# Optimization experiments

Measured on AMD Instinct MI355X. Metric: run time of the kernel, lower is better.

The kernel has to match this reference:

```python
import jax, jax.numpy as jnp
import numpy as np

B, P, D = 32, 2048, 256  # batch, patch_num, input_dim


def setup_inputs() -> dict:
    key = jax.random.key(0)
    ks = jax.random.split(key, 6)
    n = lambda k, shape: jax.random.normal(k, shape, dtype=jnp.float32) * 0.02
    return {
        "x": jax.random.normal(ks[0], (B, P, D), dtype=jnp.float32),
        "mlp_w": n(ks[1], (D, D)), "mlp_b": jnp.zeros((D,), jnp.float32),
        "his_w": n(ks[2], (D, D)), "his_b": jnp.zeros((D,), jnp.float32),
        "cur_w": n(ks[3], (D, D)), "cur_b": jnp.zeros((D,), jnp.float32),
        "wl_w": n(ks[4], (D, P)), "wl_b": jnp.zeros((P,), jnp.float32),
        "gate_w": n(ks[5], (D, 1)), "gate_b": jnp.zeros((1,), jnp.float32),
        "ln_g": jnp.ones((D,), jnp.float32), "ln_b": jnp.zeros((D,), jnp.float32),
    }


def _layernorm(h, g, b, eps=1e-5):
    mu = h.mean(-1, keepdims=True)
    var = ((h - mu) ** 2).mean(-1, keepdims=True)
    return (h - mu) * jax.lax.rsqrt(var + eps) * g + b


def reference(x, mlp_w, mlp_b, his_w, his_b, cur_w, cur_b, wl_w, wl_b,
              gate_w, gate_b, ln_g, ln_b):
    origin = x
    # expert_num == 0 -> MoE branch skipped, x unchanged
    H = origin @ his_w + his_b                              # extractor_his: [B,P,D]
    # gate(extractor_cur(origin)) -> [B,P,1], repeated along last dim == broadcast
    weight_current = (origin @ cur_w + cur_b) @ gate_w + gate_b  # [B,P,1]
    logits = H @ wl_w + wl_b                                # [B,P,P]
    weight = jax.nn.softmax(logits, axis=-1)                # row softmax
    adj = jnp.tril(weight)                                  # causal mask (diagonal=0)
    aggregated = jnp.einsum('bpq,bqd->bpd', adj, origin)    # [B,P,D]
    H_history = aggregated @ mlp_w + mlp_b                  # dropout is identity (p=0)
    H_current = weight_current * origin
    out = _layernorm(H_history + H_current, ln_g, ln_b)     # aggregated_norm == 1
    return (out, origin)
```

## Files before the change

### kernel.cpp

```cpp
#include <hip/hip_runtime.h>
#include <hip/hip_bf16.h>

typedef __attribute__((ext_vector_type(8))) short s8v;
typedef __attribute__((ext_vector_type(4))) float f4v;
typedef __attribute__((ext_vector_type(4))) unsigned int u4v;

#define BATCH 32
#define SEQ   2048
#define DIM   256
#define ORIGIN_OFF ((size_t)BATCH * SEQ * DIM)

#define XT_OFF  0ull
#define WL_OFF  16777216ull
#define HIS_OFF 17301504ull
#define MLP_OFF 17367040ull

#define BK0   0
#define BK1   32768
#define BX0   65536
#define BX1   98304
#define EP_CG 69632
#define EP_CB 70656
#define EP_WP 70672
#define EP_WC 72720

__device__ __forceinline__ unsigned short f2bf(float f) {
  __hip_bfloat16 h = __float2bfloat16(f);
  return *reinterpret_cast<unsigned short*>(&h);
}
__device__ __forceinline__ f4v mfma16(s8v a, s8v b, f4v c) {
  return __builtin_amdgcn_mfma_f32_16x16x32_bf16(a, b, c, 0, 0, 0);
}
__device__ __forceinline__ unsigned int pk2(float lo, float hi) {
  return (unsigned int)f2bf(lo) | ((unsigned int)f2bf(hi) << 16);
}
__device__ __forceinline__ void dma16(const void* g, void* l) {
  __builtin_amdgcn_global_load_lds(
      (const __attribute__((address_space(1))) unsigned int*)g,
      (__attribute__((address_space(3))) unsigned int*)l, 16, 0, 0);
}

__global__ __launch_bounds__(256) void prep_all(
    const float* __restrict__ x, const float* __restrict__ wl_w,
    const float* __restrict__ his_w, const float* __restrict__ mlp_w,
    unsigned short* __restrict__ ws)
{
  __shared__ unsigned short tile[64][72];
  const int t = threadIdx.x;
  const int tb = blockIdx.x;
  const float* src; unsigned short* dst; int lds_, ldd_, r0, c0;
  bool isx = false;
  if (tb < 4096) {
    const int b = tb >> 7, rem = tb & 127;
    r0 = (rem >> 2) * 64;  c0 = (rem & 3) * 64;
    src = x + (size_t)b * SEQ * DIM;  lds_ = DIM;
    dst = ws + XT_OFF + (size_t)b * DIM * SEQ;  ldd_ = SEQ;
    isx = true;
  } else if (tb < 4224) {
    const int t2 = tb - 4096;
    r0 = (t2 >> 5) * 64;  c0 = (t2 & 31) * 64;
    src = wl_w;  lds_ = 2048;  dst = ws + WL_OFF;  ldd_ = 256;
  } else if (tb < 4240) {
    const int t2 = tb - 4224;
    r0 = (t2 >> 2) * 64;  c0 = (t2 & 3) * 64;
    src = his_w;  lds_ = 256;  dst = ws + HIS_OFF;  ldd_ = 256;
  } else {
    const int t2 = tb - 4240;
    r0 = (t2 >> 2) * 64;  c0 = (t2 & 3) * 64;
    src = mlp_w;  lds_ = 256;  dst = ws + MLP_OFF;  ldd_ = 256;
  }
  {
    const int rr = t >> 2, cc = (t & 3) * 16;
    const float* s0 = src + (size_t)(r0 + rr) * lds_ + c0 + cc;
    f4v v0 = *(const f4v*)(s0);
    f4v v1 = *(const f4v*)(s0 + 4);
    f4v v2 = *(const f4v*)(s0 + 8);
    f4v v3 = *(const f4v*)(s0 + 12);
    u4v o0, o1;
    o0[0] = pk2(v0[0], v0[1]); o0[1] = pk2(v0[2], v0[3]);
    o0[2] = pk2(v1[0], v1[1]); o0[3] = pk2(v1[2], v1[3]);
    o1[0] = pk2(v2[0], v2[1]); o1[1] = pk2(v2[2], v2[3]);
    o1[2] = pk2(v3[0], v3[1]); o1[3] = pk2(v3[2], v3[3]);
    const int swz = rr >> 4;
    const int ch = cc >> 3;
    unsigned short* trow = &tile[rr][0];
    *(u4v*)(trow + ((ch ^ swz) << 3)) = o0;
    *(u4v*)(trow + (((ch + 1) ^ swz) << 3)) = o1;
  }
  __syncthreads();
  {
    const int cl = t >> 2, sg = t & 3;
    const int el = cl & 7;
    u4v o0, o1;
    if (isx) {
      #pragma unroll
      for (int m = 0; m < 8; ++m) {
        const int q = 32 * (sg >> 1) + 8 * (sg & 1)
                    + 16 * ((m >> 1) & 1) + 4 * (m >> 2) + 2 * (m & 1);
        const int chb = ((cl >> 3) ^ (q >> 4)) << 3;
        const unsigned int vv = (unsigned int)tile[q][chb + el]
                              | ((unsigned int)tile[q + 1][chb + el] << 16);
        if (m < 4) o0[m] = vv; else o1[m - 4] = vv;
      }
    } else {
      const int chb = ((cl >> 3) ^ sg) << 3;
      #pragma unroll
      for (int j = 0; j < 4; ++j) {
        const int rA = sg * 16 + 2 * j;
        o0[j] = (unsigned int)tile[rA][chb + el]
              | ((unsigned int)tile[rA + 1][chb + el] << 16);
      }
      #pragma unroll
      for (int j = 0; j < 4; ++j) {
        const int rA = sg * 16 + 8 + 2 * j;
        o1[j] = (unsigned int)tile[rA][chb + el]
              | ((unsigned int)tile[rA + 1][chb + el] << 16);
      }
    }
    unsigned short* d0 = dst + (size_t)(c0 + cl) * ldd_ + r0 + sg * 16;
    *(u4v*)d0 = o0;
    *(u4v*)(d0 + 8) = o1;
  }
}


__device__ __forceinline__ void gemm_stage(
    const unsigned short* __restrict__ Wt, const s8v (&af)[8],
    f4v (&acc)[16], char* smem_, int wq, int lane, int col16, int quad, int x7)
{
  char* sW = smem_ + BX1;
  const int rsub = lane >> 5;
  const int c = lane & 31;
  for (int st = 0; st < 4; ++st) {
    if (st) __syncthreads();
    #pragma unroll
    for (int j = 0; j < 4; ++j) {
      const int row = wq * 8 + 2 * j + rsub;
      dma16(Wt + (size_t)(st * 64 + row) * 256 + ((c ^ (row & 7)) << 3),
            sW + wq * 4096 + j * 1024);
    }
    __syncthreads();
    #pragma unroll
    for (int s = 0; s < 8; ++s) {
      const int co = ((s * 4 + quad) ^ x7) << 4;
      #pragma unroll
      for (int nt = 0; nt < 4; ++nt) {
        s8v bfr = *(const s8v*)(sW + (nt * 16 + col16) * 512 + co);
        acc[st * 4 + nt] = mfma16(af[s], bfr, acc[st * 4 + nt]);
      }
    }
  }
}

__global__ __launch_bounds__(512, 2)
void tfs_kernel(
    const float* __restrict__ x,
    const float* __restrict__ mlp_b,
    const float* __restrict__ his_b,
    const float* __restrict__ cur_w,
    const float* __restrict__ cur_b,
    const float* __restrict__ wl_b,
    const float* __restrict__ gate_w,
    const float* __restrict__ gate_b,
    const float* __restrict__ ln_g,
    const float* __restrict__ ln_b,
    const unsigned short* __restrict__ wsp,
    float* __restrict__ out)
{
  __shared__ __align__(16) char smem[131072];

  const int tid = threadIdx.x;
  const int lane = tid & 63;
  const int col16 = lane & 15;
  const int quad = lane >> 4;
  const int w = tid >> 6;
  const int x7 = col16 & 7;
  const int wq = __builtin_amdgcn_readfirstlane(w);

  const int b = blockIdx.y;
  const int pidx = (blockIdx.x + b) & 15;
  const int p0 = pidx * 128;
  const int pw = p0 + w * 16;
  const int pmax_qi = (p0 + 127) >> 6;

  const float* xb = x + (size_t)b * SEQ * DIM;
  const unsigned short* wlT  = wsp + WL_OFF;
  const unsigned short* hisT = wsp + HIS_OFF;
  const unsigned short* mlpT = wsp + MLP_OFF;
  const unsigned short* xTb  = wsp + XT_OFF + (size_t)b * DIM * SEQ;
  const f4v zero4 = {0.f, 0.f, 0.f, 0.f};

  s8v xf[8];
  {
    const float* srcx = xb + (size_t)(pw + col16) * DIM;
    #pragma unroll
    for (int s = 0; s < 8; ++s) {
      const int k0 = (s * 4 + quad) * 8;
      f4v v0 = *(const f4v*)(srcx + k0);
      f4v v1 = *(const f4v*)(srcx + k0 + 4);
      u4v o;
      o[0] = pk2(v0[0], v0[1]); o[1] = pk2(v0[2], v0[3]);
      o[2] = pk2(v1[0], v1[1]); o[3] = pk2(v1[2], v1[3]);
      xf[s] = *(s8v*)&o;
    }
  }

  f4v accQ[16];
  #pragma unroll
  for (int i = 0; i < 16; ++i) accQ[i] = zero4;
  gemm_stage(hisT, xf, accQ, smem, wq, lane, col16, quad, x7);
  #pragma unroll
  for (int i = 0; i < 16; ++i) {
    const int n = (i >> 2) * 64 + (i & 3) * 16 + col16;
    const float bias = his_b[n];
    #pragma unroll
    for (int r = 0; r < 4; ++r) {
      const int row = w * 16 + quad * 4 + r;
      *(unsigned short*)(smem + row * 528 + n * 2) = f2bf(accQ[i][r] + bias);
    }
  }
  __syncthreads();
  s8v qf[8];
  #pragma unroll
  for (int s = 0; s < 8; ++s)
    qf[s] = *(const s8v*)(smem + (w * 16 + col16) * 528 + (s * 4 + quad) * 16);
  __syncthreads();

  {
    const int rsub = lane >> 5, c = lane & 31;
    #pragma unroll
    for (int j = 0; j < 4; ++j) {
      const int row = wq * 8 + 2 * j + rsub;
      dma16(wlT + ((size_t)row << 8) + ((c ^ (row & 7)) << 3),
            smem + BK0 + wq * 4096 + j * 1024);
    }
    const int dsub = lane >> 3, cx = lane & 7;
    #pragma unroll
    for (int j = 0; j < 4; ++j) {
      const int d = wq * 32 + 8 * j + dsub;
      dma16(xTb + ((size_t)d << 11) + ((cx ^ dsub) << 3),
            smem + BX0 + wq * 4096 + j * 1024);
    }
  }
  __syncthreads();

  f4v accO[16];
  #pragma unroll
  for (int dt = 0; dt < 16; ++dt) accO[dt] = zero4;
  float mrun = -1.0e30f, Zrun = 0.f;

  #pragma unroll 1
  for (int qi = 0; qi < 32; ++qi) {
    const int q0 = qi * 64;
    char* bK = smem + BK0 + ((qi & 1) << 15);
    char* bX = smem + BX0 + ((qi & 1) << 15);
    char* nK = smem + BK0 + ((~qi & 1) << 15);
    char* nX = smem + BX0 + ((~qi & 1) << 15);

    if (qi < 31) {
      const int rsub = lane >> 5, c = lane & 31;
      #pragma unroll
      for (int j = 0; j < 4; ++j) {
        const int row = wq * 8 + 2 * j + rsub;
        dma16(wlT + ((size_t)(q0 + 64 + row) << 8) + ((c ^ (row & 7)) << 3),
              nK + wq * 4096 + j * 1024);
      }
      if (qi + 1 <= pmax_qi) {
        const int dsub = lane >> 3, cx = lane & 7;
        #pragma unroll
        for (int j = 0; j < 4; ++j) {
          const int d = wq * 32 + 8 * j + dsub;
          dma16(xTb + ((size_t)d << 11) + (q0 + 64) + ((cx ^ dsub) << 3),
                nX + wq * 4096 + j * 1024);
        }
      }
    }

    f4v accST[4];
    accST[0] = zero4; accST[1] = zero4; accST[2] = zero4; accST[3] = zero4;
    #pragma unroll
    for (int s = 0; s < 8; ++s) {
      const int co = ((s * 4 + quad) ^ x7) << 4;
      #pragma unroll
      for (int t = 0; t < 4; ++t) {
        s8v kf = *(const s8v*)(bK + (t * 16 + col16) * 512 + co);
        accST[t] = mfma16(kf, qf[s], accST[t]);
      }
    }
    #pragma unroll
    for (int t = 0; t < 4; ++t) {
      const f4v wb = *(const f4v*)(wl_b + q0 + t * 16 + quad * 4);
      #pragma unroll
      for (int r = 0; r < 4; ++r) accST[t][r] += wb[r];
    }
    float m01 = fmaxf(fmaxf(accST[0][0], accST[0][1]), fmaxf(accST[0][2], accST[0][3]));
    float m23 = fmaxf(fmaxf(accST[1][0], accST[1][1]), fmaxf(accST[1][2], accST[1][3]));
    float m45 = fmaxf(fmaxf(accST[2][0], accST[2][1]), fmaxf(accST[2][2], accST[2][3]));
    float m67 = fmaxf(fmaxf(accST[3][0], accST[3][1]), fmaxf(accST[3][2], accST[3][3]));
    float mt = fmaxf(fmaxf(m01, m23), fmaxf(m45, m67));
    mt = fmaxf(mt, __shfl_xor(mt, 16, 64));
    mt = fmaxf(mt, __shfl_xor(mt, 32, 64));
    const int grow = (mt > mrun) ? 1 : 0;
    const float mnew = fmaxf(mrun, mt);
    float Pv[4][4];
    #pragma unroll
    for (int t = 0; t < 4; ++t)
      #pragma unroll
      for (int r = 0; r < 4; ++r)
        Pv[t][r] = __expf(fminf(accST[t][r] - mnew, 0.f));
    float rs = 0.f;
    #pragma unroll
    for (int t = 0; t < 4; ++t)
      rs += (Pv[t][0] + Pv[t][1]) + (Pv[t][2] + Pv[t][3]);
    rs += __shfl_xor(rs, 16, 64);
    rs += __shfl_xor(rs, 32, 64);

    if (__any(grow)) {
      const float alpha = __expf(fminf(mrun - mnew, 0.f));
      float aO[4];
      #pragma unroll
      for (int r = 0; r < 4; ++r) aO[r] = __shfl(alpha, quad * 4 + r, 64);
      #pragma unroll
      for (int dt = 0; dt < 16; ++dt)
        #pragma unroll
        for (int r = 0; r < 4; ++r) accO[dt][r] *= aO[r];
      Zrun = Zrun * alpha + rs;
    } else {
      Zrun += rs;
    }
    mrun = mnew;

    if (q0 <= pw + 15) {
      const int lim = pw + col16 - q0;
      float Pm[4][4];
      #pragma unroll
      for (int t = 0; t < 4; ++t)
        #pragma unroll
        for (int r = 0; r < 4; ++r) {
          const int q = t * 16 + quad * 4 + r;
          Pm[t][r] = (q <= lim) ? Pv[t][r] : 0.f;
        }
      #pragma unroll
      for (int h = 0; h < 2; ++h) {
        u4v pw4;
        pw4[0] = pk2(Pm[2 * h][0], Pm[2 * h][1]);
        pw4[1] = pk2(Pm[2 * h][2], Pm[2 * h][3]);
        pw4[2] = pk2(Pm[2 * h + 1][0], Pm[2 * h + 1][1]);
        pw4[3] = pk2(Pm[2 * h + 1][2], Pm[2 * h + 1][3]);
        s8v pa = *(s8v*)&pw4;
        const int co = ((h * 4 + quad) ^ x7) << 4;
        #pragma unroll
        for (int dt = 0; dt < 16; ++dt) {
          const int d = dt * 16 + col16;
          s8v bv = *(const s8v*)(bX + d * 128 + co);
          accO[dt] = mfma16(pa, bv, accO[dt]);
        }
      }
    }
    __syncthreads();
  }

  float invZO[4];
  #pragma unroll
  for (int r = 0; r < 4; ++r) {
    const float z = __shfl(Zrun, quad * 4 + r, 64);
    invZO[r] = 1.0f / fmaxf(z, 1e-30f);
  }
  #pragma unroll
  for (int dt = 0; dt < 16; ++dt) {
    const int d = dt * 16 + col16;
    #pragma unroll
    for (int r = 0; r < 4; ++r) {
      const int row = w * 16 + quad * 4 + r;
      *(unsigned short*)(smem + row * 528 + d * 2) = f2bf(accO[dt][r] * invZO[r]);
    }
  }
  __syncthreads();
  s8v af[8];
  #pragma unroll
  for (int s = 0; s < 8; ++s)
    af[s] = *(const s8v*)(smem + (w * 16 + col16) * 528 + (s * 4 + quad) * 16);

  f4v accH[16];
  #pragma unroll
  for (int i = 0; i < 16; ++i) accH[i] = zero4;
  gemm_stage(mlpT, af, accH, smem, wq, lane, col16, quad, x7);

  float* cgL = (float*)(smem + EP_CG);
  float* cbL = (float*)(smem + EP_CB);
  if (tid < 256) {
    const float* cw = cur_w + (size_t)tid * DIM;
    float s = 0.f;
    #pragma unroll 8
    for (int i = 0; i < 64; ++i) {
      f4v vc = *(const f4v*)(cw + i * 4);
      f4v vg = *(const f4v*)(gate_w + i * 4);
      s += vc[0] * vg[0] + vc[1] * vg[1] + vc[2] * vg[2] + vc[3] * vg[3];
    }
    cgL[tid] = s;
    if (tid == 0) {
      float s2 = 0.f;
      for (int j = 0; j < DIM; ++j) s2 += cur_b[j] * gate_w[j];
      cbL[0] = s2 + gate_b[0];
    }
  }
  __syncthreads();

  float* wp = (float*)(smem + EP_WP);
  {
    const int row = tid >> 2, sg = tid & 3;
    const float* xr = xb + (size_t)(p0 + row) * DIM + sg * 64;
    const float* cgp = cgL + sg * 64;
    float sacc = 0.f;
    #pragma unroll
    for (int i = 0; i < 16; ++i) {
      f4v xv4 = *(const f4v*)(xr + i * 4);
      sacc += xv4[0] * cgp[i * 4] + xv4[1] * cgp[i * 4 + 1]
            + xv4[2] * cgp[i * 4 + 2] + xv4[3] * cgp[i * 4 + 3];
    }
    wp[row * 4 + sg] = sacc;
  }
  __syncthreads();
  float* wcS = (float*)(smem + EP_WC);
  if (tid < 128) {
    wcS[tid] = wp[tid * 4] + wp[tid * 4 + 1] + wp[tid * 4 + 2] + wp[tid * 4 + 3]
             + cbL[0];
  }
  __syncthreads();

  float s1l[4], s2l[4];
  #pragma unroll
  for (int r = 0; r < 4; ++r) { s1l[r] = 0.f; s2l[r] = 0.f; }
  #pragma unroll
  for (int i = 0; i < 16; ++i) {
    const int n = (i >> 2) * 64 + (i & 3) * 16 + col16;
    const float mb = mlp_b[n];
    #pragma unroll
    for (int r = 0; r < 4; ++r) {
      const int row = w * 16 + quad * 4 + r;
      const float xv = xb[(size_t)(p0 + row) * DIM + n];
      const float v = accH[i][r] + mb + wcS[row] * xv;
      accH[i][r] = v;
      s1l[r] += v;
      s2l[r] += v * v;
    }
  }
  #pragma unroll
  for (int r = 0; r < 4; ++r) {
    float v1 = s1l[r], v2 = s2l[r];
    v1 += __shfl_xor(v1, 1, 64); v2 += __shfl_xor(v2, 1, 64);
    v1 += __shfl_xor(v1, 2, 64); v2 += __shfl_xor(v2, 2, 64);
    v1 += __shfl_xor(v1, 4, 64); v2 += __shfl_xor(v2, 4, 64);
    v1 += __shfl_xor(v1, 8, 64); v2 += __shfl_xor(v2, 8, 64);
    s1l[r] = v1; s2l[r] = v2;
  }
  float mean_[4], rstd_[4];
  #pragma unroll
  for (int r = 0; r < 4; ++r) {
    const float mean = s1l[r] * (1.0f / 256.0f);
    const float var = s2l[r] * (1.0f / 256.0f) - mean * mean;
    mean_[r] = mean;
    rstd_[r] = rsqrtf(fmaxf(var, 0.f) + 1e-5f);
  }
  #pragma unroll
  for (int i = 0; i < 16; ++i) {
    const int n = (i >> 2) * 64 + (i & 3) * 16 + col16;
    const float g = ln_g[n];
    const float be = ln_b[n];
    #pragma unroll
    for (int r = 0; r < 4; ++r) {
      const int row = w * 16 + quad * 4 + r;
      const float y = (accH[i][r] - mean_[r]) * rstd_[r] * g + be;
      out[((size_t)b * SEQ + p0 + row) * DIM + n] = y;
    }
  }

  {
    const int row = tid >> 2, cs = (tid & 3) * 64;
    const float* src = xb + (size_t)(p0 + row) * DIM + cs;
    float* dst = out + ORIGIN_OFF + ((size_t)b * SEQ + p0 + row) * DIM + cs;
    #pragma unroll
    for (int j = 0; j < 16; ++j)
      *(f4v*)(dst + j * 4) = *(const f4v*)(src + j * 4);
  }
}

extern "C" void kernel_launch(void* const* d_in, const int* in_sizes, int n_in,
                              void* d_out, int out_size, void* d_ws, size_t ws_size,
                              hipStream_t stream) {
  const float* x      = (const float*)d_in[0];
  const float* mlp_w  = (const float*)d_in[1];
  const float* mlp_b  = (const float*)d_in[2];
  const float* his_w  = (const float*)d_in[3];
  const float* his_b  = (const float*)d_in[4];
  const float* cur_w  = (const float*)d_in[5];
  const float* cur_b  = (const float*)d_in[6];
  const float* wl_w   = (const float*)d_in[7];
  const float* wl_b   = (const float*)d_in[8];
  const float* gate_w = (const float*)d_in[9];
  const float* gate_b = (const float*)d_in[10];
  const float* ln_g   = (const float*)d_in[11];
  const float* ln_b   = (const float*)d_in[12];

  unsigned short* ws = (unsigned short*)d_ws;

  prep_all<<<dim3(4256), 256, 0, stream>>>(x, wl_w, his_w, mlp_w, ws);
  tfs_kernel<<<dim3(16, 32), 512, 0, stream>>>(
      x, mlp_b, his_b, cur_w, cur_b, wl_b, gate_w, gate_b,
      ln_g, ln_b, ws, (float*)d_out);
}
```

Baseline: 448.3 us.

## Defer P·X MFMA by one tile to overlap with next score MFMAs

Software-pipelines the attention-style loop. The probability fragments of each key tile are kept in registers, and their P·X MFMAs are issued in the next iteration right after the score MFMAs, with a final drain after the loop. The X tile is now loaded into the current buffer and consumed one iteration later, so the softmax-to-PV dependency no longer stalls the matrix units. In exchange it holds two extra fragment registers and adds an epilogue, and correctness relies on the deferred add happening before the running-max rescale.

```diff
diff --git a/kernel.cpp b/kernel.cpp
--- a/kernel.cpp
+++ b/kernel.cpp
@@ -234,13 +234,6 @@
       dma16(wlT + ((size_t)row << 8) + ((c ^ (row & 7)) << 3),
             smem + BK0 + wq * 4096 + j * 1024);
     }
-    const int dsub = lane >> 3, cx = lane & 7;
-    #pragma unroll
-    for (int j = 0; j < 4; ++j) {
-      const int d = wq * 32 + 8 * j + dsub;
-      dma16(xTb + ((size_t)d << 11) + ((cx ^ dsub) << 3),
-            smem + BX0 + wq * 4096 + j * 1024);
-    }
   }
   __syncthreads();
 
@@ -248,14 +241,16 @@
   #pragma unroll
   for (int dt = 0; dt < 16; ++dt) accO[dt] = zero4;
   float mrun = -1.0e30f, Zrun = 0.f;
+  s8v paA[2];
+  paA[0] = (s8v)(short)0; paA[1] = (s8v)(short)0;
 
   #pragma unroll 1
   for (int qi = 0; qi < 32; ++qi) {
     const int q0 = qi * 64;
     char* bK = smem + BK0 + ((qi & 1) << 15);
-    char* bX = smem + BX0 + ((qi & 1) << 15);
     char* nK = smem + BK0 + ((~qi & 1) << 15);
-    char* nX = smem + BX0 + ((~qi & 1) << 15);
+    char* cX = smem + BX0 + ((qi & 1) << 15);
+    char* pX = smem + BX0 + ((~qi & 1) << 15);
 
     if (qi < 31) {
       const int rsub = lane >> 5, c = lane & 31;
@@ -265,14 +260,14 @@
         dma16(wlT + ((size_t)(q0 + 64 + row) << 8) + ((c ^ (row & 7)) << 3),
               nK + wq * 4096 + j * 1024);
       }
-      if (qi + 1 <= pmax_qi) {
-        const int dsub = lane >> 3, cx = lane & 7;
-        #pragma unroll
-        for (int j = 0; j < 4; ++j) {
-          const int d = wq * 32 + 8 * j + dsub;
-          dma16(xTb + ((size_t)d << 11) + (q0 + 64) + ((cx ^ dsub) << 3),
-                nX + wq * 4096 + j * 1024);
-        }
+    }
+    if (qi <= pmax_qi) {
+      const int dsub = lane >> 3, cx = lane & 7;
+      #pragma unroll
+      for (int j = 0; j < 4; ++j) {
+        const int d = wq * 32 + 8 * j + dsub;
+        dma16(xTb + ((size_t)d << 11) + q0 + ((cx ^ dsub) << 3),
+              cX + wq * 4096 + j * 1024);
       }
     }
 
@@ -287,6 +282,20 @@
         accST[t] = mfma16(kf, qf[s], accST[t]);
       }
     }
+
+    if (qi > 0 && (q0 - 64) <= pw + 15) {
+      #pragma unroll
+      for (int h = 0; h < 2; ++h) {
+        const int co = ((h * 4 + quad) ^ x7) << 4;
+        #pragma unroll
+        for (int dt = 0; dt < 16; ++dt) {
+          const int d = dt * 16 + col16;
+          s8v bv = *(const s8v*)(pX + d * 128 + co);
+          accO[dt] = mfma16(paA[h], bv, accO[dt]);
+        }
+      }
+    }
+
     #pragma unroll
     for (int t = 0; t < 4; ++t) {
       const f4v wb = *(const f4v*)(wl_b + q0 + t * 16 + quad * 4);
@@ -347,17 +356,24 @@
         pw4[1] = pk2(Pm[2 * h][2], Pm[2 * h][3]);
         pw4[2] = pk2(Pm[2 * h + 1][0], Pm[2 * h + 1][1]);
         pw4[3] = pk2(Pm[2 * h + 1][2], Pm[2 * h + 1][3]);
-        s8v pa = *(s8v*)&pw4;
-        const int co = ((h * 4 + quad) ^ x7) << 4;
-        #pragma unroll
-        for (int dt = 0; dt < 16; ++dt) {
-          const int d = dt * 16 + col16;
-          s8v bv = *(const s8v*)(bX + d * 128 + co);
-          accO[dt] = mfma16(pa, bv, accO[dt]);
-        }
+        paA[h] = *(s8v*)&pw4;
       }
     }
     __syncthreads();
+  }
+
+  if (1984 <= pw + 15) {
+    char* pX = smem + BX0 + (1 << 15);
+    #pragma unroll
+    for (int h = 0; h < 2; ++h) {
+      const int co = ((h * 4 + quad) ^ x7) << 4;
+      #pragma unroll
+      for (int dt = 0; dt < 16; ++dt) {
+        const int d = dt * 16 + col16;
+        s8v bv = *(const s8v*)(pX + d * 128 + co);
+        accO[dt] = mfma16(paA[h], bv, accO[dt]);
+      }
+    }
   }
 
   float invZO[4];
```

New measurement: 459.5 us. 2.5% more time.

## Switch fused attention kernel to 32x32x16 MFMA with 4 waves and smaller tiles

Applied to the files above, without the earlier changes.

Replaces the 16x16x32 bf16 MFMA tiles with 32x32x16 MFMA throughout: the his and mlp GEMMs, the logits computation and the P·X accumulation. Each wave now owns 32 rows, the block drops to 256 threads, the K/X stream step shrinks from 64 to 32 columns, and LDS use halves to 64KB. The prep kernel's transposed-x layout and the LDS swizzles are reworked to match the new fragment layout. The aim is fewer MFMA issues and fewer LDS fragment reads per FLOP. The cost is more accumulator registers per thread and more loop iterations with a barrier each, so occupancy may suffer.

```diff
diff --git a/kernel.cpp b/kernel.cpp
--- a/kernel.cpp
+++ b/kernel.cpp
@@ -3,6 +3,7 @@
 
 typedef __attribute__((ext_vector_type(8))) short s8v;
 typedef __attribute__((ext_vector_type(4))) float f4v;
+typedef __attribute__((ext_vector_type(16))) float f16v;
 typedef __attribute__((ext_vector_type(4))) unsigned int u4v;
 
 #define BATCH 32
@@ -15,21 +16,18 @@
 #define HIS_OFF 17301504ull
 #define MLP_OFF 17367040ull
 
-#define BK0   0
-#define BK1   32768
-#define BX0   65536
-#define BX1   98304
-#define EP_CG 69632
-#define EP_CB 70656
-#define EP_WP 70672
-#define EP_WC 72720
+#define BX0   32768
+#define WST   32768
+#define EP_CB 1024
+#define EP_WP 1040
+#define EP_WC 2064
 
 __device__ __forceinline__ unsigned short f2bf(float f) {
   __hip_bfloat16 h = __float2bfloat16(f);
   return *reinterpret_cast<unsigned short*>(&h);
 }
-__device__ __forceinline__ f4v mfma16(s8v a, s8v b, f4v c) {
-  return __builtin_amdgcn_mfma_f32_16x16x32_bf16(a, b, c, 0, 0, 0);
+__device__ __forceinline__ f16v mfma32(s8v a, s8v b, f16v c) {
+  return __builtin_amdgcn_mfma_f32_32x32x16_bf16(a, b, c, 0, 0, 0);
 }
 __device__ __forceinline__ unsigned int pk2(float lo, float hi) {
   return (unsigned int)f2bf(lo) | ((unsigned int)f2bf(hi) << 16);
@@ -91,19 +89,24 @@
   {
     const int cl = t >> 2, sg = t & 3;
     const int el = cl & 7;
+    const int chb = ((cl >> 3) ^ sg) << 3;
     u4v o0, o1;
     if (isx) {
-      #pragma unroll
-      for (int m = 0; m < 8; ++m) {
-        const int q = 32 * (sg >> 1) + 8 * (sg & 1)
-                    + 16 * ((m >> 1) & 1) + 4 * (m >> 2) + 2 * (m & 1);
-        const int chb = ((cl >> 3) ^ (q >> 4)) << 3;
-        const unsigned int vv = (unsigned int)tile[q][chb + el]
-                              | ((unsigned int)tile[q + 1][chb + el] << 16);
-        if (m < 4) o0[m] = vv; else o1[m - 4] = vv;
+      const int pe0[4] = {0, 2, 8, 10};
+      const int pe1[4] = {4, 6, 12, 14};
+      #pragma unroll
+      for (int j = 0; j < 4; ++j) {
+        const int rA = sg * 16 + pe0[j];
+        o0[j] = (unsigned int)tile[rA][chb + el]
+              | ((unsigned int)tile[rA + 1][chb + el] << 16);
+      }
+      #pragma unroll
+      for (int j = 0; j < 4; ++j) {
+        const int rA = sg * 16 + pe1[j];
+        o1[j] = (unsigned int)tile[rA][chb + el]
+              | ((unsigned int)tile[rA + 1][chb + el] << 16);
       }
     } else {
-      const int chb = ((cl >> 3) ^ sg) << 3;
       #pragma unroll
       for (int j = 0; j < 4; ++j) {
         const int rA = sg * 16 + 2 * j;
@@ -124,35 +127,34 @@
 }
 
 
-__device__ __forceinline__ void gemm_stage(
-    const unsigned short* __restrict__ Wt, const s8v (&af)[8],
-    f4v (&acc)[16], char* smem_, int wq, int lane, int col16, int quad, int x7)
+__device__ __forceinline__ void gemm_stage32(
+    const unsigned short* __restrict__ Wt, const s8v (&af)[16],
+    f16v (&acc)[8], char* smem_, int wq, int lane)
 {
-  char* sW = smem_ + BX1;
-  const int rsub = lane >> 5;
-  const int c = lane & 31;
+  char* sW = smem_ + WST;
+  const int hi = lane >> 5, l31 = lane & 31, l7 = lane & 7;
   for (int st = 0; st < 4; ++st) {
     if (st) __syncthreads();
     #pragma unroll
-    for (int j = 0; j < 4; ++j) {
-      const int row = wq * 8 + 2 * j + rsub;
-      dma16(Wt + (size_t)(st * 64 + row) * 256 + ((c ^ (row & 7)) << 3),
-            sW + wq * 4096 + j * 1024);
+    for (int j = 0; j < 8; ++j) {
+      const int row = wq * 16 + 2 * j + hi;
+      dma16(Wt + (size_t)(st * 64 + row) * 256 + ((l31 ^ (row & 7)) << 3),
+            sW + wq * 8192 + j * 1024);
     }
     __syncthreads();
     #pragma unroll
-    for (int s = 0; s < 8; ++s) {
-      const int co = ((s * 4 + quad) ^ x7) << 4;
-      #pragma unroll
-      for (int nt = 0; nt < 4; ++nt) {
-        s8v bfr = *(const s8v*)(sW + (nt * 16 + col16) * 512 + co);
-        acc[st * 4 + nt] = mfma16(af[s], bfr, acc[st * 4 + nt]);
-      }
-    }
-  }
-}
-
-__global__ __launch_bounds__(512, 2)
+    for (int ks = 0; ks < 16; ++ks) {
+      #pragma unroll
+      for (int nt = 0; nt < 2; ++nt) {
+        s8v bfr = *(const s8v*)(sW + (nt * 32 + l31) * 512
+                                + (((ks * 2 + hi) ^ l7) << 4));
+        acc[st * 2 + nt] = mfma32(af[ks], bfr, acc[st * 2 + nt]);
+      }
+    }
+  }
+}
+
+__global__ __launch_bounds__(256, 2)
 void tfs_kernel(
     const float* __restrict__ x,
     const float* __restrict__ mlp_b,
@@ -167,228 +169,235 @@
     const unsigned short* __restrict__ wsp,
     float* __restrict__ out)
 {
-  __shared__ __align__(16) char smem[131072];
+  __shared__ __align__(16) char smem[65536];
 
   const int tid = threadIdx.x;
   const int lane = tid & 63;
-  const int col16 = lane & 15;
-  const int quad = lane >> 4;
+  const int l31 = lane & 31;
+  const int hi = lane >> 5;
+  const int l7 = lane & 7;
   const int w = tid >> 6;
-  const int x7 = col16 & 7;
   const int wq = __builtin_amdgcn_readfirstlane(w);
 
   const int b = blockIdx.y;
   const int pidx = (blockIdx.x + b) & 15;
   const int p0 = pidx * 128;
-  const int pw = p0 + w * 16;
-  const int pmax_qi = (p0 + 127) >> 6;
+  const int pw = p0 + w * 32;
+  const int pcol = pw + l31;
+  const int qimax = (p0 + 127) >> 5;
 
   const float* xb = x + (size_t)b * SEQ * DIM;
   const unsigned short* wlT  = wsp + WL_OFF;
   const unsigned short* hisT = wsp + HIS_OFF;
   const unsigned short* mlpT = wsp + MLP_OFF;
   const unsigned short* xTb  = wsp + XT_OFF + (size_t)b * DIM * SEQ;
-  const f4v zero4 = {0.f, 0.f, 0.f, 0.f};
-
-  s8v xf[8];
-  {
-    const float* srcx = xb + (size_t)(pw + col16) * DIM;
-    #pragma unroll
-    for (int s = 0; s < 8; ++s) {
-      const int k0 = (s * 4 + quad) * 8;
+
+  s8v xf[16];
+  {
+    const float* srcx = xb + (size_t)pcol * DIM;
+    #pragma unroll
+    for (int ks = 0; ks < 16; ++ks) {
+      const int k0 = ks * 16 + hi * 8;
       f4v v0 = *(const f4v*)(srcx + k0);
       f4v v1 = *(const f4v*)(srcx + k0 + 4);
       u4v o;
       o[0] = pk2(v0[0], v0[1]); o[1] = pk2(v0[2], v0[3]);
       o[2] = pk2(v1[0], v1[1]); o[3] = pk2(v1[2], v1[3]);
-      xf[s] = *(s8v*)&o;
-    }
-  }
-
-  f4v accQ[16];
-  #pragma unroll
-  for (int i = 0; i < 16; ++i) accQ[i] = zero4;
-  gemm_stage(hisT, xf, accQ, smem, wq, lane, col16, quad, x7);
-  #pragma unroll
-  for (int i = 0; i < 16; ++i) {
-    const int n = (i >> 2) * 64 + (i & 3) * 16 + col16;
+      xf[ks] = *(s8v*)&o;
+    }
+  }
+
+  f16v accQ[8];
+  #pragma unroll
+  for (int i = 0; i < 8; ++i)
+    #pragma unroll
+    for (int e = 0; e < 16; ++e) accQ[i][e] = 0.f;
+  gemm_stage32(hisT, xf, accQ, smem, wq, lane);
+  __syncthreads();
+  #pragma unroll
+  for (int i = 0; i < 8; ++i) {
+    const int n = i * 32 + l31;
     const float bias = his_b[n];
     #pragma unroll
-    for (int r = 0; r < 4; ++r) {
-      const int row = w * 16 + quad * 4 + r;
-      *(unsigned short*)(smem + row * 528 + n * 2) = f2bf(accQ[i][r] + bias);
-    }
-  }
-  __syncthreads();
-  s8v qf[8];
-  #pragma unroll
-  for (int s = 0; s < 8; ++s)
-    qf[s] = *(const s8v*)(smem + (w * 16 + col16) * 528 + (s * 4 + quad) * 16);
-  __syncthreads();
-
-  {
-    const int rsub = lane >> 5, c = lane & 31;
+    for (int r = 0; r < 16; ++r) {
+      const int ploc = w * 32 + (r & 3) + 8 * (r >> 2) + 4 * hi;
+      const int slot = (n >> 3) ^ (ploc & 7);
+      *(unsigned short*)(smem + ploc * 512 + slot * 16 + (n & 7) * 2)
+          = f2bf(accQ[i][r] + bias);
+    }
+  }
+  __syncthreads();
+  s8v qf[16];
+  #pragma unroll
+  for (int ks = 0; ks < 16; ++ks)
+    qf[ks] = *(const s8v*)(smem + (w * 32 + l31) * 512
+                           + (((ks * 2 + hi) ^ l7) << 4));
+  __syncthreads();
+
+  {
     #pragma unroll
     for (int j = 0; j < 4; ++j) {
-      const int row = wq * 8 + 2 * j + rsub;
-      dma16(wlT + ((size_t)row << 8) + ((c ^ (row & 7)) << 3),
-            smem + BK0 + wq * 4096 + j * 1024);
-    }
-    const int dsub = lane >> 3, cx = lane & 7;
+      const int q = wq * 8 + 2 * j + hi;
+      dma16(wlT + ((size_t)q << 8) + ((l31 ^ (q & 7)) << 3),
+            smem + wq * 4096 + j * 1024);
+    }
+    const int dr = lane >> 2, cx = lane & 3;
     #pragma unroll
     for (int j = 0; j < 4; ++j) {
-      const int d = wq * 32 + 8 * j + dsub;
-      dma16(xTb + ((size_t)d << 11) + ((cx ^ dsub) << 3),
+      const int d = wq * 64 + j * 16 + dr;
+      dma16(xTb + ((size_t)d << 11) + ((cx ^ ((d >> 1) & 3)) << 3),
             smem + BX0 + wq * 4096 + j * 1024);
     }
   }
   __syncthreads();
 
-  f4v accO[16];
-  #pragma unroll
-  for (int dt = 0; dt < 16; ++dt) accO[dt] = zero4;
+  f16v accO[8];
+  #pragma unroll
+  for (int dt = 0; dt < 8; ++dt)
+    #pragma unroll
+    for (int e = 0; e < 16; ++e) accO[dt][e] = 0.f;
   float mrun = -1.0e30f, Zrun = 0.f;
 
   #pragma unroll 1
-  for (int qi = 0; qi < 32; ++qi) {
-    const int q0 = qi * 64;
-    char* bK = smem + BK0 + ((qi & 1) << 15);
-    char* bX = smem + BX0 + ((qi & 1) << 15);
-    char* nK = smem + BK0 + ((~qi & 1) << 15);
-    char* nX = smem + BX0 + ((~qi & 1) << 15);
-
-    if (qi < 31) {
-      const int rsub = lane >> 5, c = lane & 31;
+  for (int qi = 0; qi < 64; ++qi) {
+    const int q0 = qi * 32;
+    char* bK = smem + ((qi & 1) << 14);
+    char* nK = smem + ((~qi & 1) << 14);
+    char* bX = smem + BX0 + ((qi & 1) << 14);
+    char* nX = smem + BX0 + ((~qi & 1) << 14);
+
+    if (qi < 63) {
       #pragma unroll
       for (int j = 0; j < 4; ++j) {
-        const int row = wq * 8 + 2 * j + rsub;
-        dma16(wlT + ((size_t)(q0 + 64 + row) << 8) + ((c ^ (row & 7)) << 3),
+        const int q = wq * 8 + 2 * j + hi;
+        dma16(wlT + ((size_t)(q0 + 32 + q) << 8) + ((l31 ^ (q & 7)) << 3),
               nK + wq * 4096 + j * 1024);
       }
-      if (qi + 1 <= pmax_qi) {
-        const int dsub = lane >> 3, cx = lane & 7;
+      if (qi + 1 <= qimax) {
+        const int dr = lane >> 2, cx = lane & 3;
         #pragma unroll
         for (int j = 0; j < 4; ++j) {
-          const int d = wq * 32 + 8 * j + dsub;
-          dma16(xTb + ((size_t)d << 11) + (q0 + 64) + ((cx ^ dsub) << 3),
+          const int d = wq * 64 + j * 16 + dr;
+          dma16(xTb + ((size_t)d << 11) + (q0 + 32)
+                    + ((cx ^ ((d >> 1) & 3)) << 3),
                 nX + wq * 4096 + j * 1024);
         }
       }
     }
 
-    f4v accST[4];
-    accST[0] = zero4; accST[1] = zero4; accST[2] = zero4; accST[3] = zero4;
-    #pragma unroll
-    for (int s = 0; s < 8; ++s) {
-      const int co = ((s * 4 + quad) ^ x7) << 4;
-      #pragma unroll
-      for (int t = 0; t < 4; ++t) {
-        s8v kf = *(const s8v*)(bK + (t * 16 + col16) * 512 + co);
-        accST[t] = mfma16(kf, qf[s], accST[t]);
-      }
-    }
-    #pragma unroll
-    for (int t = 0; t < 4; ++t) {
-      const f4v wb = *(const f4v*)(wl_b + q0 + t * 16 + quad * 4);
-      #pragma unroll
-      for (int r = 0; r < 4; ++r) accST[t][r] += wb[r];
-    }
-    float m01 = fmaxf(fmaxf(accST[0][0], accST[0][1]), fmaxf(accST[0][2], accST[0][3]));
-    float m23 = fmaxf(fmaxf(accST[1][0], accST[1][1]), fmaxf(accST[1][2], accST[1][3]));
-    float m45 = fmaxf(fmaxf(accST[2][0], accST[2][1]), fmaxf(accST[2][2], accST[2][3]));
-    float m67 = fmaxf(fmaxf(accST[3][0], accST[3][1]), fmaxf(accST[3][2], accST[3][3]));
-    float mt = fmaxf(fmaxf(m01, m23), fmaxf(m45, m67));
-    mt = fmaxf(mt, __shfl_xor(mt, 16, 64));
+    f16v a0, a1;
+    #pragma unroll
+    for (int e = 0; e < 16; ++e) { a0[e] = 0.f; a1[e] = 0.f; }
+    #pragma unroll
+    for (int ks = 0; ks < 16; ks += 2) {
+      s8v kf0 = *(const s8v*)(bK + l31 * 512 + (((ks * 2 + hi) ^ l7) << 4));
+      s8v kf1 = *(const s8v*)(bK + l31 * 512 + ((((ks + 1) * 2 + hi) ^ l7) << 4));
+      a0 = mfma32(kf0, qf[ks], a0);
+      a1 = mfma32(kf1, qf[ks + 1], a1);
+    }
+    float S[16];
+    #pragma unroll
+    for (int j2 = 0; j2 < 4; ++j2) {
+      const f4v wb = *(const f4v*)(wl_b + q0 + 8 * j2 + 4 * hi);
+      #pragma unroll
+      for (int c = 0; c < 4; ++c)
+        S[j2 * 4 + c] = a0[j2 * 4 + c] + a1[j2 * 4 + c] + wb[c];
+    }
+    float mt = S[0];
+    #pragma unroll
+    for (int r = 1; r < 16; ++r) mt = fmaxf(mt, S[r]);
     mt = fmaxf(mt, __shfl_xor(mt, 32, 64));
     const int grow = (mt > mrun) ? 1 : 0;
     const float mnew = fmaxf(mrun, mt);
-    float Pv[4][4];
-    #pragma unroll
-    for (int t = 0; t < 4; ++t)
-      #pragma unroll
-      for (int r = 0; r < 4; ++r)
-        Pv[t][r] = __expf(fminf(accST[t][r] - mnew, 0.f));
+    #pragma unroll
+    for (int r = 0; r < 16; ++r)
+      S[r] = __expf(fminf(S[r] - mnew, 0.f));
     float rs = 0.f;
     #pragma unroll
-    for (int t = 0; t < 4; ++t)
-      rs += (Pv[t][0] + Pv[t][1]) + (Pv[t][2] + Pv[t][3]);
-    rs += __shfl_xor(rs, 16, 64);
+    for (int r = 0; r < 16; ++r) rs += S[r];
     rs += __shfl_xor(rs, 32, 64);
 
     if (__any(grow)) {
       const float alpha = __expf(fminf(mrun - mnew, 0.f));
-      float aO[4];
-      #pragma unroll
-      for (int r = 0; r < 4; ++r) aO[r] = __shfl(alpha, quad * 4 + r, 64);
-      #pragma unroll
-      for (int dt = 0; dt < 16; ++dt)
+      float aR[16];
+      #pragma unroll
+      for (int r = 0; r < 16; ++r)
+        aR[r] = __shfl(alpha, (r & 3) + 8 * (r >> 2) + 4 * hi, 64);
+      #pragma unroll
+      for (int dt = 0; dt < 8; ++dt)
         #pragma unroll
-        for (int r = 0; r < 4; ++r) accO[dt][r] *= aO[r];
+        for (int r = 0; r < 16; ++r) accO[dt][r] *= aR[r];
       Zrun = Zrun * alpha + rs;
     } else {
       Zrun += rs;
     }
     mrun = mnew;
 
-    if (q0 <= pw + 15) {
-      const int lim = pw + col16 - q0;
-      float Pm[4][4];
-      #pragma unroll
-      for (int t = 0; t < 4; ++t)
+    if (q0 <= pw + 31) {
+      #pragma unroll
+      for (int r = 0; r < 16; ++r) {
+        const int qg = q0 + (r & 3) + 8 * (r >> 2) + 4 * hi;
+        S[r] = (qg <= pcol) ? S[r] : 0.f;
+      }
+      s8v pa[2];
+      #pragma unroll
+      for (int w2 = 0; w2 < 2; ++w2) {
+        u4v pk;
+        pk[0] = pk2(S[8 * w2 + 0], S[8 * w2 + 1]);
+        pk[1] = pk2(S[8 * w2 + 2], S[8 * w2 + 3]);
+        pk[2] = pk2(S[8 * w2 + 4], S[8 * w2 + 5]);
+        pk[3] = pk2(S[8 * w2 + 6], S[8 * w2 + 7]);
+        pa[w2] = *(s8v*)&pk;
+      }
+      #pragma unroll
+      for (int w2 = 0; w2 < 2; ++w2) {
         #pragma unroll
-        for (int r = 0; r < 4; ++r) {
-          const int q = t * 16 + quad * 4 + r;
-          Pm[t][r] = (q <= lim) ? Pv[t][r] : 0.f;
+        for (int dt = 0; dt < 8; ++dt) {
+          const int d = dt * 32 + l31;
+          s8v bv = *(const s8v*)(bX + d * 64
+                    + (((w2 * 2 + hi) ^ ((d >> 1) & 3)) << 4));
+          accO[dt] = mfma32(pa[w2], bv, accO[dt]);
         }
-      #pragma unroll
-      for (int h = 0; h < 2; ++h) {
-        u4v pw4;
-        pw4[0] = pk2(Pm[2 * h][0], Pm[2 * h][1]);
-        pw4[1] = pk2(Pm[2 * h][2], Pm[2 * h][3]);
-        pw4[2] = pk2(Pm[2 * h + 1][0], Pm[2 * h + 1][1]);
-        pw4[3] = pk2(Pm[2 * h + 1][2], Pm[2 * h + 1][3]);
-        s8v pa = *(s8v*)&pw4;
-        const int co = ((h * 4 + quad) ^ x7) << 4;
-        #pragma unroll
-        for (int dt = 0; dt < 16; ++dt) {
-          const int d = dt * 16 + col16;
-          s8v bv = *(const s8v*)(bX + d * 128 + co);
-          accO[dt] = mfma16(pa, bv, accO[dt]);
-        }
       }
     }
     __syncthreads();
   }
 
-  float invZO[4];
-  #pragma unroll
-  for (int r = 0; r < 4; ++r) {
-    const float z = __shfl(Zrun, quad * 4 + r, 64);
-    invZO[r] = 1.0f / fmaxf(z, 1e-30f);
-  }
-  #pragma unroll
-  for (int dt = 0; dt < 16; ++dt) {
-    const int d = dt * 16 + col16;
-    #pragma unroll
-    for (int r = 0; r < 4; ++r) {
-      const int row = w * 16 + quad * 4 + r;
-      *(unsigned short*)(smem + row * 528 + d * 2) = f2bf(accO[dt][r] * invZO[r]);
-    }
-  }
-  __syncthreads();
-  s8v af[8];
-  #pragma unroll
-  for (int s = 0; s < 8; ++s)
-    af[s] = *(const s8v*)(smem + (w * 16 + col16) * 528 + (s * 4 + quad) * 16);
-
-  f4v accH[16];
-  #pragma unroll
-  for (int i = 0; i < 16; ++i) accH[i] = zero4;
-  gemm_stage(mlpT, af, accH, smem, wq, lane, col16, quad, x7);
-
-  float* cgL = (float*)(smem + EP_CG);
+  float izR[16];
+  #pragma unroll
+  for (int r = 0; r < 16; ++r) {
+    const float z = __shfl(Zrun, (r & 3) + 8 * (r >> 2) + 4 * hi, 64);
+    izR[r] = 1.0f / fmaxf(z, 1e-30f);
+  }
+  #pragma unroll
+  for (int dt = 0; dt < 8; ++dt) {
+    const int d = dt * 32 + l31;
+    #pragma unroll
+    for (int r = 0; r < 16; ++r) {
+      const int ploc = w * 32 + (r & 3) + 8 * (r >> 2) + 4 * hi;
+      const int slot = (d >> 3) ^ (ploc & 7);
+      *(unsigned short*)(smem + ploc * 512 + slot * 16 + (d & 7) * 2)
+          = f2bf(accO[dt][r] * izR[r]);
+    }
+  }
+  __syncthreads();
+  s8v af[16];
+  #pragma unroll
+  for (int ks = 0; ks < 16; ++ks)
+    af[ks] = *(const s8v*)(smem + (w * 32 + l31) * 512
+                           + (((ks * 2 + hi) ^ l7) << 4));
+  __syncthreads();
+
+  f16v accH[8];
+  #pragma unroll
+  for (int i = 0; i < 8; ++i)
+    #pragma unroll
+    for (int e = 0; e < 16; ++e) accH[i][e] = 0.f;
+  gemm_stage32(mlpT, af, accH, smem, wq, lane);
+
+  float* cgL = (float*)(smem);
   float* cbL = (float*)(smem + EP_CB);
-  if (tid < 256) {
+  {
     const float* cw = cur_w + (size_t)tid * DIM;
     float s = 0.f;
     #pragma unroll 8
@@ -408,79 +417,80 @@
 
   float* wp = (float*)(smem + EP_WP);
   {
-    const int row = tid >> 2, sg = tid & 3;
-    const float* xr = xb + (size_t)(p0 + row) * DIM + sg * 64;
-    const float* cgp = cgL + sg * 64;
+    const int row = tid >> 1, sg = tid & 1;
+    const float* xr = xb + (size_t)(p0 + row) * DIM + sg * 128;
+    const float* cgp = cgL + sg * 128;
     float sacc = 0.f;
     #pragma unroll
-    for (int i = 0; i < 16; ++i) {
+    for (int i = 0; i < 32; ++i) {
       f4v xv4 = *(const f4v*)(xr + i * 4);
       sacc += xv4[0] * cgp[i * 4] + xv4[1] * cgp[i * 4 + 1]
             + xv4[2] * cgp[i * 4 + 2] + xv4[3] * cgp[i * 4 + 3];
     }
-    wp[row * 4 + sg] = sacc;
+    wp[row * 2 + sg] = sacc;
   }
   __syncthreads();
   float* wcS = (float*)(smem + EP_WC);
   if (tid < 128) {
-    wcS[tid] = wp[tid * 4] + wp[tid * 4 + 1] + wp[tid * 4 + 2] + wp[tid * 4 + 3]
-             + cbL[0];
-  }
-  __syncthreads();
-
-  float s1l[4], s2l[4];
-  #pragma unroll
-  for (int r = 0; r < 4; ++r) { s1l[r] = 0.f; s2l[r] = 0.f; }
-  #pragma unroll
-  for (int i = 0; i < 16; ++i) {
-    const int n = (i >> 2) * 64 + (i & 3) * 16 + col16;
-    const float mb = mlp_b[n];
-    #pragma unroll
-    for (int r = 0; r < 4; ++r) {
-      const int row = w * 16 + quad * 4 + r;
-      const float xv = xb[(size_t)(p0 + row) * DIM + n];
-      const float v = accH[i][r] + mb + wcS[row] * xv;
+    wcS[tid] = wp[tid * 2] + wp[tid * 2 + 1] + cbL[0];
+  }
+  __syncthreads();
+
+  float mb8[8], g8[8], be8[8];
+  #pragma unroll
+  for (int i = 0; i < 8; ++i) {
+    const int n = i * 32 + l31;
+    mb8[i] = mlp_b[n];
+    g8[i] = ln_g[n];
+    be8[i] = ln_b[n];
+  }
+  float s1l[16], s2l[16];
+  #pragma unroll
+  for (int r = 0; r < 16; ++r) {
+    const int ploc = w * 32 + (r & 3) + 8 * (r >> 2) + 4 * hi;
+    const float wc_ = wcS[ploc];
+    const float* xrow = xb + (size_t)(p0 + ploc) * DIM;
+    float s1 = 0.f, s2 = 0.f;
+    #pragma unroll
+    for (int i = 0; i < 8; ++i) {
+      const float xv = xrow[i * 32 + l31];
+      const float v = accH[i][r] + mb8[i] + wc_ * xv;
       accH[i][r] = v;
-      s1l[r] += v;
-      s2l[r] += v * v;
-    }
-  }
-  #pragma unroll
-  for (int r = 0; r < 4; ++r) {
+      s1 += v;
+      s2 += v * v;
+    }
+    s1l[r] = s1; s2l[r] = s2;
+  }
+  #pragma unroll
+  for (int r = 0; r < 16; ++r) {
     float v1 = s1l[r], v2 = s2l[r];
-    v1 += __shfl_xor(v1, 1, 64); v2 += __shfl_xor(v2, 1, 64);
-    v1 += __shfl_xor(v1, 2, 64); v2 += __shfl_xor(v2, 2, 64);
-    v1 += __shfl_xor(v1, 4, 64); v2 += __shfl_xor(v2, 4, 64);
-    v1 += __shfl_xor(v1, 8, 64); v2 += __shfl_xor(v2, 8, 64);
+    v1 += __shfl_xor(v1, 1, 64);  v2 += __shfl_xor(v2, 1, 64);
+    v1 += __shfl_xor(v1, 2, 64);  v2 += __shfl_xor(v2, 2, 64);
+    v1 += __shfl_xor(v1, 4, 64);  v2 += __shfl_xor(v2, 4, 64);
+    v1 += __shfl_xor(v1, 8, 64);  v2 += __shfl_xor(v2, 8, 64);
+    v1 += __shfl_xor(v1, 16, 64); v2 += __shfl_xor(v2, 16, 64);
     s1l[r] = v1; s2l[r] = v2;
   }
-  float mean_[4], rstd_[4];
-  #pragma unroll
-  for (int r = 0; r < 4; ++r) {
+  #pragma unroll
+  for (int r = 0; r < 16; ++r) {
+    const int ploc = w * 32 + (r & 3) + 8 * (r >> 2) + 4 * hi;
     const float mean = s1l[r] * (1.0f / 256.0f);
     const float var = s2l[r] * (1.0f / 256.0f) - mean * mean;
-    mean_[r] = mean;
-    rstd_[r] = rsqrtf(fmaxf(var, 0.f) + 1e-5f);
-  }
-  #pragma unroll
-  for (int i = 0; i < 16; ++i) {
-    const int n = (i >> 2) * 64 + (i & 3) * 16 + col16;
-    const float g = ln_g[n];
-    const float be = ln_b[n];
-    #pragma unroll
-    for (int r = 0; r < 4; ++r) {
-      const int row = w * 16 + quad * 4 + r;
-      const float y = (accH[i][r] - mean_[r]) * rstd_[r] * g + be;
-      out[((size_t)b * SEQ + p0 + row) * DIM + n] = y;
-    }
-  }
-
-  {
-    const int row = tid >> 2, cs = (tid & 3) * 64;
+    const float rstd = rsqrtf(fmaxf(var, 0.f) + 1e-5f);
+    float* orow = out + ((size_t)b * SEQ + p0 + ploc) * DIM;
+    #pragma unroll
+    for (int i = 0; i < 8; ++i) {
+      const float y = (accH[i][r] - mean) * rstd * g8[i] + be8[i];
+      orow[i * 32 + l31] = y;
+    }
+  }
+
+  {
+    const int row = tid >> 1, cs = (tid & 1) * 128;
     const float* src = xb + (size_t)(p0 + row) * DIM + cs;
     float* dst = out + ORIGIN_OFF + ((size_t)b * SEQ + p0 + row) * DIM + cs;
     #pragma unroll
-    for (int j = 0; j < 16; ++j)
+    for (int j = 0; j < 32; ++j)
       *(f4v*)(dst + j * 4) = *(const f4v*)(src + j * 4);
   }
 }
@@ -505,7 +515,7 @@
   unsigned short* ws = (unsigned short*)d_ws;
 
   prep_all<<<dim3(4256), 256, 0, stream>>>(x, wl_w, his_w, mlp_w, ws);
-  tfs_kernel<<<dim3(16, 32), 512, 0, stream>>>(
+  tfs_kernel<<<dim3(16, 32), 256, 0, stream>>>(
       x, mlp_b, his_b, cur_w, cur_b, wl_b, gate_w, gate_b,
       ln_g, ln_b, ws, (float*)d_out);
 }
```

Result: slower. 701.7 us (+56.5%).
